# Kernel optimization log

Hardware: AMD Instinct MI355X
Metric: run time of the kernel (lower is better)

The kernel has to match this reference:

```python
import jax, jax.numpy as jnp
import numpy as np

N = 8192
E = 262144
FEAT = 512
HID = 512
OUT = 64


def gcn_conv(x, src, dst, W, b, num_nodes):
    # PyG GCNConv: add self-loops, symmetric deg^-1/2 normalization,
    # message = norm * (x @ W)[src], aggregated at dst, plus bias.
    loop = jnp.arange(num_nodes)
    s = jnp.concatenate([src, loop])
    d = jnp.concatenate([dst, loop])
    deg = jax.ops.segment_sum(jnp.ones_like(d, dtype=x.dtype), d, num_segments=num_nodes)
    dinv = jnp.where(deg > 0, deg ** -0.5, 0.0)
    norm = dinv[s] * dinv[d]                      # [E+N]
    h = x @ W                                      # [N, hid]
    msg = h[s] * norm[:, None]                     # gather + scale
    out = jax.ops.segment_sum(msg, d, num_segments=num_nodes)
    return out + b


def feature_dis(x):
    # cosine-similarity matrix with zeroed diagonal (get_feature_dis)
    n = x.shape[0]
    x_dis = x @ x.T                                # [N, N]
    s = jnp.sqrt(jnp.sum(x * x, axis=1, keepdims=True))  # [N, 1]
    x_sum = s @ s.T
    x_sum = jnp.where(x_sum == 0, jnp.asarray(1e-8, x.dtype), x_sum)
    x_dis = x_dis / x_sum
    return x_dis * (1.0 - jnp.eye(n, dtype=x.dtype))


def setup_inputs() -> dict:
    key = jax.random.key(0)
    ks = jax.random.split(key, 6)
    x = jax.random.normal(ks[0], (N, FEAT), dtype=jnp.float32)
    edge_index = jax.random.randint(ks[1], (2, E), 0, N)
    W1 = jax.random.normal(ks[2], (FEAT, HID), dtype=jnp.float32) * (1.0 / np.sqrt(FEAT))
    b1 = jnp.zeros((HID,), dtype=jnp.float32)
    W2 = jax.random.normal(ks[3], (HID, HID), dtype=jnp.float32) * (1.0 / np.sqrt(HID))
    b2 = jnp.zeros((HID,), dtype=jnp.float32)
    fcW = jax.random.normal(ks[4], (HID, OUT), dtype=jnp.float32) * (1.0 / np.sqrt(HID))
    fcb = jnp.zeros((OUT,), dtype=jnp.float32)
    return {"x": x, "edge_index": edge_index, "W1": W1, "b1": b1,
            "W2": W2, "b2": b2, "fcW": fcW, "fcb": fcb}


def reference(x, edge_index, W1, b1, W2, b2, fcW, fcb):
    src, dst = edge_index[0], edge_index[1]
    n = x.shape[0]
    h = jax.nn.relu(gcn_conv(x, src, dst, W1, b1, n))
    # dropout p=0.0 / eval mode -> identity
    h = gcn_conv(h, src, dst, W2, b2, n)
    x_hid = jax.nn.relu(h)
    x_dis = feature_dis(x_hid)
    logits = x_hid @ fcW + fcb
    return (logits, x_dis)
```

## Files before the change

kernel.cpp:

```cpp
#include <hip/hip_runtime.h>

#define N_NODES 8192
#define N_EDGES 262144
#define FEAT    512
#define HIDDIM  512
#define NOUT    64

typedef short bf16x8 __attribute__((ext_vector_type(8)));
typedef float f32x4  __attribute__((ext_vector_type(4)));

__device__ __forceinline__ unsigned short f2bf(float f) {
  unsigned int u = __float_as_uint(f);
  u += 0x7fffu + ((u >> 16) & 1u);
  return (unsigned short)(u >> 16);
}
__device__ __forceinline__ float bf2f(unsigned short h) {
  return __uint_as_float(((unsigned int)h) << 16);
}
__device__ __forceinline__ float lo2f(unsigned int v) { return __uint_as_float(v << 16); }
__device__ __forceinline__ float hi2f(unsigned int v) { return __uint_as_float(v & 0xffff0000u); }
__device__ __forceinline__ unsigned int packbf(float a, float b) {
  return (unsigned int)f2bf(a) | ((unsigned int)f2bf(b) << 16);
}

__device__ __forceinline__ void async_copy16(const unsigned short* g, unsigned short* l) {
  __builtin_amdgcn_global_load_lds(
      (const __attribute__((address_space(1))) unsigned int*)g,
      (__attribute__((address_space(3))) unsigned int*)l, 16, 0, 0);
}

__global__ void cast4_k(const float* __restrict__ in, unsigned int* __restrict__ out, int n4) {
  int i = blockIdx.x * blockDim.x + threadIdx.x;
  if (i >= n4) return;
  float4 v = ((const float4*)in)[i];
  out[2 * i]     = packbf(v.x, v.y);
  out[2 * i + 1] = packbf(v.z, v.w);
}

__global__ void tcast_k(const float* __restrict__ in, unsigned short* __restrict__ out, int R, int C) {
  __shared__ float tile[32][33];
  int bx = blockIdx.x * 32;
  int by = blockIdx.y * 32;
  int tx = threadIdx.x, ty = threadIdx.y;
#pragma unroll
  for (int j = 0; j < 32; j += 8)
    tile[ty + j][tx] = in[(size_t)(by + ty + j) * C + bx + tx];
  __syncthreads();
#pragma unroll
  for (int j = 0; j < 32; j += 8)
    out[(size_t)(bx + ty + j) * R + by + tx] = f2bf(tile[tx][ty + j]);
}

__global__ void init_k(int* __restrict__ deg, int* __restrict__ cursor) {
  int i = blockIdx.x * blockDim.x + threadIdx.x;
  if (i < N_NODES) { deg[i] = 1; cursor[i] = 0; }
}
__global__ void count_k(const int* __restrict__ dst, int* __restrict__ deg) {
  for (int i = blockIdx.x * blockDim.x + threadIdx.x; i < N_EDGES; i += gridDim.x * blockDim.x)
    atomicAdd(&deg[dst[i]], 1);
}
__global__ void dinv_k(const int* __restrict__ deg, float* __restrict__ dinv) {
  int i = blockIdx.x * blockDim.x + threadIdx.x;
  if (i < N_NODES) dinv[i] = rsqrtf((float)deg[i]);
}
__global__ __launch_bounds__(1024) void scan_k(const int* __restrict__ deg, int* __restrict__ offs) {
  __shared__ int sums[1024];
  int tid = threadIdx.x;
  int vals[8]; int s = 0;
#pragma unroll
  for (int k = 0; k < 8; k++) { vals[k] = deg[tid * 8 + k] - 1; s += vals[k]; }
  sums[tid] = s;
  __syncthreads();
  for (int off = 1; off < 1024; off <<= 1) {
    int add = (tid >= off) ? sums[tid - off] : 0;
    __syncthreads();
    sums[tid] += add;
    __syncthreads();
  }
  int prefix = (tid > 0) ? sums[tid - 1] : 0;
#pragma unroll
  for (int k = 0; k < 8; k++) { offs[tid * 8 + k] = prefix; prefix += vals[k]; }
  if (tid == 1023) offs[N_NODES] = prefix;
}
__global__ void scatter_k(const int* __restrict__ src, const int* __restrict__ dst,
                          const int* __restrict__ offs, int* __restrict__ cursor,
                          const float* __restrict__ dinv,
                          int* __restrict__ ssrc, float* __restrict__ enorm) {
  for (int i = blockIdx.x * blockDim.x + threadIdx.x; i < N_EDGES; i += gridDim.x * blockDim.x) {
    int s = src[i], d = dst[i];
    int pos = offs[d] + atomicAdd(&cursor[d], 1);
    ssrc[pos]  = s;
    enorm[pos] = dinv[s] * dinv[d];
  }
}

template <bool OUT_BF16, bool ZERO_DIAG>
__global__ __launch_bounds__(256) void gemm_bt(
    const unsigned short* __restrict__ A, const unsigned short* __restrict__ B,
    void* __restrict__ Cout, int M, int Ncols, int K) {
  __shared__ unsigned short lA[128 * 32];
  __shared__ unsigned short lB[128 * 32];
  const int tid  = threadIdx.x;
  const int lane = tid & 63, w = tid >> 6;
  const int wm = w >> 1, wn = w & 1;
  const int lm = lane & 15, q = lane >> 4;
  const int bm = blockIdx.y * 128, bn = blockIdx.x * 128;

  f32x4 acc[4][4];
#pragma unroll
  for (int r = 0; r < 4; r++)
#pragma unroll
    for (int c = 0; c < 4; c++) acc[r][c] = (f32x4){0.f, 0.f, 0.f, 0.f};

  const int rowOff = tid >> 2;
  const int kOff   = (tid & 3) * 8;
  const unsigned short* gA0 = A + (size_t)(bm + rowOff) * K + kOff;
  const unsigned short* gA1 = gA0 + (size_t)64 * K;
  const unsigned short* gB0 = B + (size_t)(bn + rowOff) * K + kOff;
  const unsigned short* gB1 = gB0 + (size_t)64 * K;
  unsigned short* lAw = lA + w * 512;
  unsigned short* lBw = lB + w * 512;

  for (int k0 = 0; k0 < K; k0 += 32) {
    async_copy16(gA0 + k0, lAw);
    async_copy16(gA1 + k0, lAw + 2048);
    async_copy16(gB0 + k0, lBw);
    async_copy16(gB1 + k0, lBw + 2048);
    asm volatile("s_waitcnt vmcnt(0)" ::: "memory");
    __syncthreads();

    bf16x8 av[4], bv[4];
#pragma unroll
    for (int r = 0; r < 4; r++)
      av[r] = *(const bf16x8*)&lA[(wm * 64 + r * 16 + lm) * 32 + q * 8];
#pragma unroll
    for (int c = 0; c < 4; c++)
      bv[c] = *(const bf16x8*)&lB[(wn * 64 + c * 16 + lm) * 32 + q * 8];
#pragma unroll
    for (int r = 0; r < 4; r++)
#pragma unroll
      for (int c = 0; c < 4; c++)
        acc[r][c] = __builtin_amdgcn_mfma_f32_16x16x32_bf16(av[r], bv[c], acc[r][c], 0, 0, 0);
    __syncthreads();
  }

  const int grow0 = bm + wm * 64 + q * 4;
  const int gcol0 = bn + wn * 64 + lm;
#pragma unroll
  for (int r = 0; r < 4; r++) {
#pragma unroll
    for (int c = 0; c < 4; c++) {
      int col = gcol0 + c * 16;
#pragma unroll
      for (int v = 0; v < 4; v++) {
        int row = grow0 + r * 16 + v;
        float val = acc[r][c][v];
        if (ZERO_DIAG && row == col) val = 0.f;
        if (OUT_BF16)
          ((unsigned short*)Cout)[(size_t)row * Ncols + col] = f2bf(val);
        else
          ((float*)Cout)[(size_t)row * Ncols + col] = val;
      }
    }
  }
}

template <bool NORM>
__global__ __launch_bounds__(256) void aggregate_k(
    const unsigned int* __restrict__ Hu,
    const int* __restrict__ offs, const int* __restrict__ ssrc,
    const float* __restrict__ enorm, const float* __restrict__ dinv,
    const float* __restrict__ bias,
    unsigned int* __restrict__ outU, unsigned int* __restrict__ yU) {
  const int i = blockIdx.x;
  const int tid = threadIdx.x;
  __shared__ int   sS[256];
  __shared__ float sN[256];
  __shared__ float wsum[4];

  float di = dinv[i];
  unsigned int hv = Hu[(size_t)i * 256 + tid];
  float ax = lo2f(hv) * di * di;
  float ay = hi2f(hv) * di * di;

  int e0 = offs[i], e1 = offs[i + 1];
  for (int base = e0; base < e1; base += 256) {
    int n = min(256, e1 - base);
    if (tid < n) { sS[tid] = ssrc[base + tid]; sN[tid] = enorm[base + tid]; }
    __syncthreads();
    int j = 0;
    for (; j + 4 <= n; j += 4) {
      int s0 = sS[j], s1 = sS[j + 1], s2 = sS[j + 2], s3 = sS[j + 3];
      float n0 = sN[j], n1 = sN[j + 1], n2 = sN[j + 2], n3 = sN[j + 3];
      unsigned int v0 = Hu[(size_t)s0 * 256 + tid];
      unsigned int v1 = Hu[(size_t)s1 * 256 + tid];
      unsigned int v2 = Hu[(size_t)s2 * 256 + tid];
      unsigned int v3 = Hu[(size_t)s3 * 256 + tid];
      ax = fmaf(n0, lo2f(v0), ax); ay = fmaf(n0, hi2f(v0), ay);
      ax = fmaf(n1, lo2f(v1), ax); ay = fmaf(n1, hi2f(v1), ay);
      ax = fmaf(n2, lo2f(v2), ax); ay = fmaf(n2, hi2f(v2), ay);
      ax = fmaf(n3, lo2f(v3), ax); ay = fmaf(n3, hi2f(v3), ay);
    }
    for (; j < n; j++) {
      int s = sS[j]; float nw = sN[j];
      unsigned int v = Hu[(size_t)s * 256 + tid];
      ax = fmaf(nw, lo2f(v), ax); ay = fmaf(nw, hi2f(v), ay);
    }
    __syncthreads();
  }

  float rx = fmaxf(ax + bias[tid * 2],     0.f);
  float ry = fmaxf(ay + bias[tid * 2 + 1], 0.f);
  outU[(size_t)i * 256 + tid] = packbf(rx, ry);

  if (NORM) {
    float ss = rx * rx + ry * ry;
    for (int o = 32; o > 0; o >>= 1) ss += __shfl_down(ss, o);
    if ((tid & 63) == 0) wsum[tid >> 6] = ss;
    __syncthreads();
    float tot = wsum[0] + wsum[1] + wsum[2] + wsum[3];
    float rn = tot > 0.f ? 1.f / sqrtf(tot) : 0.f;
    yU[(size_t)i * 256 + tid] = packbf(rx * rn, ry * rn);
  }
}

__global__ __launch_bounds__(256) void logits_k(
    const unsigned short* __restrict__ xh,
    const unsigned short* __restrict__ fw,
    const float* __restrict__ fcb, float* __restrict__ out) {
  __shared__ unsigned short sX[512 * 4];
  int tid = threadIdx.x;
  int rowBase = blockIdx.x * 4;
  for (int idx = tid; idx < 2048; idx += 256) {
    int r = idx >> 9, k = idx & 511;
    sX[k * 4 + r] = xh[(size_t)(rowBase + r) * 512 + k];
  }
  __syncthreads();
  int c = tid & 63, r = tid >> 6;
  float acc = 0.f;
#pragma unroll 8
  for (int k = 0; k < 512; k++)
    acc = fmaf(bf2f(sX[k * 4 + r]), bf2f(fw[(size_t)k * 64 + c]), acc);
  out[(size_t)(rowBase + r) * 64 + c] = acc + fcb[c];
}

extern "C" void kernel_launch(void* const* d_in, const int* in_sizes, int n_in,
                              void* d_out, int out_size, void* d_ws, size_t ws_size,
                              hipStream_t stream) {
  const float* x   = (const float*)d_in[0];
  const int*   ei  = (const int*)d_in[1];
  const float* W1  = (const float*)d_in[2];
  const float* b1  = (const float*)d_in[3];
  const float* W2  = (const float*)d_in[4];
  const float* b2  = (const float*)d_in[5];
  const float* fcW = (const float*)d_in[6];
  const float* fcb = (const float*)d_in[7];
  const int* src = ei;
  const int* dst = ei + N_EDGES;

  float* logits = (float*)d_out;
  float* xdis   = logits + (size_t)N_NODES * NOUT;

  char* p = (char*)d_ws;
  auto alloc = [&](size_t bytes) { char* r = p; p += (bytes + 255) & ~(size_t)255; return r; };
  unsigned short* xb   = (unsigned short*)alloc((size_t)N_NODES * FEAT * 2);
  unsigned short* hb   = (unsigned short*)alloc((size_t)N_NODES * HIDDIM * 2);
  unsigned short* h1b  = (unsigned short*)alloc((size_t)N_NODES * HIDDIM * 2);
  unsigned short* xhb  = (unsigned short*)alloc((size_t)N_NODES * HIDDIM * 2);
  unsigned short* yb   = (unsigned short*)alloc((size_t)N_NODES * HIDDIM * 2);
  unsigned short* w1t  = (unsigned short*)alloc((size_t)FEAT * HIDDIM * 2);
  unsigned short* w2t  = (unsigned short*)alloc((size_t)HIDDIM * HIDDIM * 2);
  unsigned short* fwb  = (unsigned short*)alloc((size_t)HIDDIM * NOUT * 2);
  int*   deg    = (int*)alloc(N_NODES * 4);
  float* dinv   = (float*)alloc(N_NODES * 4);
  int*   offs   = (int*)alloc((N_NODES + 1) * 4);
  int*   cursor = (int*)alloc(N_NODES * 4);
  int*   ssrc   = (int*)alloc(N_EDGES * 4);
  float* enorm  = (float*)alloc(N_EDGES * 4);

  cast4_k<<<(N_NODES * FEAT / 4 + 255) / 256, 256, 0, stream>>>(x, (unsigned int*)xb, N_NODES * FEAT / 4);
  tcast_k<<<dim3(HIDDIM / 32, FEAT / 32), dim3(32, 8), 0, stream>>>(W1, w1t, FEAT, HIDDIM);
  tcast_k<<<dim3(HIDDIM / 32, HIDDIM / 32), dim3(32, 8), 0, stream>>>(W2, w2t, HIDDIM, HIDDIM);
  cast4_k<<<(HIDDIM * NOUT / 4 + 255) / 256, 256, 0, stream>>>(fcW, (unsigned int*)fwb, HIDDIM * NOUT / 4);

  init_k<<<N_NODES / 256, 256, 0, stream>>>(deg, cursor);
  count_k<<<256, 256, 0, stream>>>(dst, deg);
  dinv_k<<<N_NODES / 256, 256, 0, stream>>>(deg, dinv);
  scan_k<<<1, 1024, 0, stream>>>(deg, offs);
  scatter_k<<<256, 256, 0, stream>>>(src, dst, offs, cursor, dinv, ssrc, enorm);

  gemm_bt<true, false><<<dim3(HIDDIM / 128, N_NODES / 128), 256, 0, stream>>>(xb, w1t, hb, N_NODES, HIDDIM, FEAT);
  aggregate_k<false><<<N_NODES, 256, 0, stream>>>((const unsigned int*)hb, offs, ssrc, enorm, dinv, b1,
                                                  (unsigned int*)h1b, nullptr);
  gemm_bt<true, false><<<dim3(HIDDIM / 128, N_NODES / 128), 256, 0, stream>>>(h1b, w2t, hb, N_NODES, HIDDIM, HIDDIM);
  aggregate_k<true><<<N_NODES, 256, 0, stream>>>((const unsigned int*)hb, offs, ssrc, enorm, dinv, b2,
                                                 (unsigned int*)xhb, (unsigned int*)yb);

  logits_k<<<N_NODES / 4, 256, 0, stream>>>(xhb, fwb, fcb, logits);

  gemm_bt<false, true><<<dim3(N_NODES / 128, N_NODES / 128), 256, 0, stream>>>(yb, yb, xdis, N_NODES, N_NODES, HIDDIM);
}
```

Measured before the change: 518.9 us.

## Compute only lower-triangular tiles of symmetric similarity matrix and mirror via LDS

Replaces the full N×N Y·Yᵀ GEMM with a triangular launch that computes each off-diagonal 128×128 tile once. The transpose is written to the mirrored tile through an LDS transpose with vectorized stores. This halves MFMA work and input loads, but the full output still has to be written, and the extra LDS staging and syncs are added per tile.

```diff
diff --git a/kernel.cpp b/kernel.cpp
--- a/kernel.cpp
+++ b/kernel.cpp
@@ -162,6 +162,107 @@
           ((float*)Cout)[(size_t)row * Ncols + col] = val;
       }
     }
+  }
+}
+
+__global__ __launch_bounds__(256) void gemm_sym(
+    const unsigned short* __restrict__ Y, float* __restrict__ C) {
+  __shared__ __align__(16) char smem[64 * 132 * 4];
+  unsigned short* lA = (unsigned short*)smem;
+  unsigned short* lB = (unsigned short*)(smem + 8192);
+  float* ldsT = (float*)smem;
+
+  const int t = blockIdx.x;
+  int bi = (int)((sqrtf(8.0f * t + 1.0f) - 1.0f) * 0.5f);
+  while ((bi + 1) * (bi + 2) / 2 <= t) bi++;
+  while (bi * (bi + 1) / 2 > t) bi--;
+  const int bj = t - bi * (bi + 1) / 2;
+
+  const int tid  = threadIdx.x;
+  const int lane = tid & 63, w = tid >> 6;
+  const int wm = w >> 1, wn = w & 1;
+  const int lm = lane & 15, q = lane >> 4;
+  const int bm = bi * 128, bn = bj * 128;
+  const int K = HIDDIM;
+
+  f32x4 acc[4][4];
+#pragma unroll
+  for (int r = 0; r < 4; r++)
+#pragma unroll
+    for (int c = 0; c < 4; c++) acc[r][c] = (f32x4){0.f, 0.f, 0.f, 0.f};
+
+  const int rowOff = tid >> 2;
+  const int kOff   = (tid & 3) * 8;
+  const unsigned short* gA0 = Y + (size_t)(bm + rowOff) * K + kOff;
+  const unsigned short* gA1 = gA0 + (size_t)64 * K;
+  const unsigned short* gB0 = Y + (size_t)(bn + rowOff) * K + kOff;
+  const unsigned short* gB1 = gB0 + (size_t)64 * K;
+  unsigned short* lAw = lA + w * 512;
+  unsigned short* lBw = lB + w * 512;
+
+  for (int k0 = 0; k0 < K; k0 += 32) {
+    async_copy16(gA0 + k0, lAw);
+    async_copy16(gA1 + k0, lAw + 2048);
+    async_copy16(gB0 + k0, lBw);
+    async_copy16(gB1 + k0, lBw + 2048);
+    asm volatile("s_waitcnt vmcnt(0)" ::: "memory");
+    __syncthreads();
+
+    bf16x8 av[4], bv[4];
+#pragma unroll
+    for (int r = 0; r < 4; r++)
+      av[r] = *(const bf16x8*)&lA[(wm * 64 + r * 16 + lm) * 32 + q * 8];
+#pragma unroll
+    for (int c = 0; c < 4; c++)
+      bv[c] = *(const bf16x8*)&lB[(wn * 64 + c * 16 + lm) * 32 + q * 8];
+#pragma unroll
+    for (int r = 0; r < 4; r++)
+#pragma unroll
+      for (int c = 0; c < 4; c++)
+        acc[r][c] = __builtin_amdgcn_mfma_f32_16x16x32_bf16(av[r], bv[c], acc[r][c], 0, 0, 0);
+    __syncthreads();
+  }
+
+  const int grow0 = bm + wm * 64 + q * 4;
+  const int gcol0 = bn + wn * 64 + lm;
+#pragma unroll
+  for (int r = 0; r < 4; r++) {
+#pragma unroll
+    for (int c = 0; c < 4; c++) {
+      int col = gcol0 + c * 16;
+#pragma unroll
+      for (int v = 0; v < 4; v++) {
+        int row = grow0 + r * 16 + v;
+        float val = acc[r][c][v];
+        if (bi == bj && row == col) val = 0.f;
+        C[(size_t)row * N_NODES + col] = val;
+      }
+    }
+  }
+
+  if (bi == bj) return;
+
+#pragma unroll
+  for (int h = 0; h < 2; h++) {
+    __syncthreads();
+    if (wn == h) {
+#pragma unroll
+      for (int r = 0; r < 4; r++)
+#pragma unroll
+        for (int c = 0; c < 4; c++) {
+          int lcol = c * 16 + lm;
+          int lrow = wm * 64 + r * 16 + q * 4;
+          *(f32x4*)&ldsT[lcol * 132 + lrow] = acc[r][c];
+        }
+    }
+    __syncthreads();
+    const int cl = tid >> 2;
+    const int cc = (tid & 3) * 32;
+    float* drow = C + (size_t)(bn + h * 64 + cl) * N_NODES + bm + cc;
+    const float* srow = &ldsT[cl * 132 + cc];
+#pragma unroll
+    for (int j = 0; j < 32; j += 4)
+      *(float4*)&drow[j] = *(const float4*)&srow[j];
   }
 }
 
@@ -298,5 +399,5 @@
 
   logits_k<<<N_NODES / 4, 256, 0, stream>>>(xhb, fwb, fcb, logits);
 
-  gemm_bt<false, true><<<dim3(N_NODES / 128, N_NODES / 128), 256, 0, stream>>>(yb, yb, xdis, N_NODES, N_NODES, HIDDIM);
-}
+  gemm_sym<<<2080, 256, 0, stream>>>(yb, xdis);
+}
```

New measurement: 538.8 us. 3.8% more time.
